# Performance work log

Measured on AMD Instinct MI355X. Metric: run time of the kernel, lower is better.

Reference implementation:

```python
import jax, jax.numpy as jnp
import numpy as np

B, K, BIN = 16, 2048, 256
GRU, EMB, HID = 1024, 1024, 1024
H, KV = 16, 4
D = HID // H          # 64 head dim
NREP = H // KV        # 4 GQA repeat factor


def rotate_half(x):
    x1, x2 = jnp.split(x, 2, axis=-1)
    return jnp.concatenate((-x2, x1), axis=-1)


def setup_inputs() -> dict:
    key = jax.random.key(0)
    ks = jax.random.split(key, 8)
    h = jax.random.normal(ks[0], (B, K, GRU), dtype=jnp.float32)
    # real RoPE frequency tables, shape (BIN, D)
    inv_freq = 1.0 / (10000.0 ** (jnp.arange(0, D, 2, dtype=jnp.float32) / D))
    t = jnp.arange(BIN, dtype=jnp.float32)
    freqs = jnp.outer(t, inv_freq)                      # (BIN, D/2)
    emb = jnp.concatenate((freqs, freqs), axis=-1)      # (BIN, D)
    freqs_cos, freqs_sin = jnp.cos(emb), jnp.sin(emb)
    s = lambda fan: 1.0 / np.sqrt(fan).astype(np.float32)
    Wq = jax.random.normal(ks[1], (H * D, EMB), jnp.float32) * s(EMB)
    Wk = jax.random.normal(ks[2], (KV * D, GRU), jnp.float32) * s(GRU)
    Wv = jax.random.normal(ks[3], (KV * D, GRU), jnp.float32) * s(GRU)
    Wo = jax.random.normal(ks[4], (EMB, H * D), jnp.float32) * s(H * D)
    output_queries = jax.random.normal(ks[5], (BIN, EMB), jnp.float32)
    Wr = jax.random.normal(ks[6], (2, EMB), jnp.float32) * s(EMB)
    br = jnp.zeros((2,), jnp.float32)
    return {"h": h, "freqs_cos": freqs_cos, "freqs_sin": freqs_sin,
            "Wq": Wq, "Wk": Wk, "Wv": Wv, "Wo": Wo,
            "output_queries": output_queries, "Wr": Wr, "br": br}


def reference(h, freqs_cos, freqs_sin, Wq, Wk, Wv, Wo, output_queries, Wr, br):
    # KV projections from GRU history: (B, K, KV, D)
    k = (h @ Wk.T).reshape(B, K, KV, D)
    v = (h @ Wv.T).reshape(B, K, KV, D)
    # Queries are batch-invariant learned tokens: (BIN, H, D)
    q = (output_queries @ Wq.T).reshape(BIN, H, D)
    cos = freqs_cos[:, None, :]  # (BIN, 1, D) broadcast over heads
    sin = freqs_sin[:, None, :]
    q = q * cos + rotate_half(q) * sin
    # GQA: repeat_interleave KV heads to H heads
    k_rep = jnp.repeat(k, NREP, axis=2)  # (B, K, H, D)
    v_rep = jnp.repeat(v, NREP, axis=2)
    scores = jnp.einsum('qhd,bkhd->bhqk', q, k_rep) / np.sqrt(D).astype(np.float32)
    attn = jax.nn.softmax(scores, axis=-1)               # dropout p=0 (eval)
    out = jnp.einsum('bhqk,bkhd->bqhd', attn, v_rep).reshape(B, BIN, H * D)
    z = out @ Wo.T                                        # (B, BIN, EMB)
    return z @ Wr.T + br                                  # (B, BIN, 2)
```

## Files before the change

### kernel.cpp

```cpp
#include <hip/hip_runtime.h>

typedef __attribute__((ext_vector_type(8))) short short8;
typedef __attribute__((ext_vector_type(4))) float f32x4;
typedef __attribute__((ext_vector_type(16))) float f32x16;

#define DEV static __device__ __forceinline__

DEV unsigned short f2bf(float f) {
  unsigned int u = __float_as_uint(f);
  u += 0x7fff + ((u >> 16) & 1);
  return (unsigned short)(u >> 16);
}

DEV unsigned int cvtpk(float lo, float hi) {
  unsigned int r;
  asm("v_cvt_pk_bf16_f32 %0, %1, %2" : "=v"(r) : "v"(lo), "v"(hi));
  return r;
}

DEV float max3f(float a, float b, float c) {
  float r;
  asm("v_max3_f32 %0, %1, %2, %3" : "=v"(r) : "v"(a), "v"(b), "v"(c));
  return r;
}

DEV f32x4 mfma16(short8 a, short8 b, f32x4 c) {
  return __builtin_amdgcn_mfma_f32_16x16x32_bf16(a, b, c, 0, 0, 0);
}

DEV f32x16 mfma32(short8 a, short8 b, f32x16 c) {
  return __builtin_amdgcn_mfma_f32_32x32x16_bf16(a, b, c, 0, 0, 0);
}

DEV void gl_lds16(const void* g, void* l) {
  __builtin_amdgcn_global_load_lds((const __attribute__((address_space(1))) void*)g,
                                   (__attribute__((address_space(3))) void*)l, 16, 0, 0);
}

__global__ __launch_bounds__(256) void cvtB_kernel(const float* __restrict__ Wq,
                                                   const float* __restrict__ Wk,
                                                   const float* __restrict__ Wv,
                                                   unsigned short* __restrict__ wqb,
                                                   unsigned short* __restrict__ wkvb) {
  int id = blockIdx.x * 256 + threadIdx.x;
  int e = id * 4;
  float4 v;
  unsigned short* d;
  if (e < 1048576)      { v = *(const float4*)(Wq + e);             d = wqb + e; }
  else if (e < 1310720) { v = *(const float4*)(Wk + (e - 1048576)); d = wkvb + (e - 1048576); }
  else                  { v = *(const float4*)(Wv + (e - 1310720)); d = wkvb + 262144 + (e - 1310720); }
  uint2 pk;
  pk.x = cvtpk(v.x, v.y);
  pk.y = cvtpk(v.z, v.w);
  *(uint2*)d = pk;
}

__global__ __launch_bounds__(256) void wrp_partial(const float* __restrict__ Wr,
                                                   const float* __restrict__ Wo,
                                                   float* __restrict__ part) {
  int blk = blockIdx.x;
  int tid = threadIdx.x;
  float a0[4] = {0.f,0.f,0.f,0.f};
  float a1[4] = {0.f,0.f,0.f,0.f};
  int e0 = blk * 64;
  for (int e = e0; e < e0 + 64; e++) {
    float w0 = Wr[e];
    float w1 = Wr[1024 + e];
    #pragma unroll
    for (int j4 = 0; j4 < 4; j4++) {
      float wo = Wo[(size_t)e * 1024 + j4 * 256 + tid];
      a0[j4] += w0 * wo;
      a1[j4] += w1 * wo;
    }
  }
  #pragma unroll
  for (int j4 = 0; j4 < 4; j4++) {
    part[blk * 2048 + 0    + j4 * 256 + tid] = a0[j4];
    part[blk * 2048 + 1024 + j4 * 256 + tid] = a1[j4];
  }
}

__global__ __launch_bounds__(256) void wrp_reduce(const float* __restrict__ part,
                                                  float* __restrict__ Wrp) {
  int id = blockIdx.x * 256 + threadIdx.x;
  float s = 0.f;
  #pragma unroll
  for (int blk = 0; blk < 16; blk++) s += part[blk * 2048 + id];
  Wrp[id] = s;
}

__global__ __launch_bounds__(512, 2) void gemm_kv(const float* __restrict__ A,
                                                  const unsigned short* __restrict__ Bb,
                                                  unsigned short* __restrict__ ok,
                                                  unsigned short* __restrict__ vrm) {
  __shared__ unsigned short Asl[3][4096];
  __shared__ unsigned short Bsl[3][16384];

  int bid = blockIdx.x;
  int sw = (bid & 7) * 32 + (bid >> 3);
  int m0 = sw * 128;

  int tid = threadIdx.x;
  int w = tid >> 6, l = tid & 63;
  int l4 = l >> 4, l15 = l & 15;

  int arow = tid >> 2, ac = tid & 3;
  const float* ga = A + (size_t)(m0 + arow) * 1024 + ac * 8;
  int awb = arow * 64 + ((ac ^ ((arow >> 1) & 3)) * 16);

  const unsigned short* gbB = Bb + (size_t)(tid >> 2) * 1024
                                 + (((tid & 3) ^ ((tid >> 3) & 3)) * 8);

  int fsw = (l4 ^ ((l15 >> 1) & 3)) * 16;
  int aoff = l15 * 64 + fsw;
  int boff = (w * 64 + l15) * 64 + fsw;

  f32x4 acc[8][4];
  #pragma unroll
  for (int i = 0; i < 8; i++)
    #pragma unroll
    for (int j = 0; j < 4; j++) acc[i][j] = (f32x4)(0.f);

  float4 aXx, aXy, aYx, aYy;

  #define LOADA(T, RX, RY)                                                  \
    { const float* gA = ga + (T) * 32;                                      \
      RX = *(const float4*)(gA);                                            \
      RY = *(const float4*)(gA + 4); }

  #define STAGEB(SB, T)                                                     \
    { const unsigned short* b0p = gbB + (T) * 32;                           \
      gl_lds16(b0p,          (char*)Bsl[SB] + tid * 16);                    \
      gl_lds16(b0p + 131072, (char*)Bsl[SB] + 8192  + tid * 16);            \
      gl_lds16(b0p + 262144, (char*)Bsl[SB] + 16384 + tid * 16);            \
      gl_lds16(b0p + 393216, (char*)Bsl[SB] + 24576 + tid * 16); }

  #define WRITEA(WB, RX, RY)                                                \
    { union { short8 s; unsigned int u[4]; } af;                            \
      af.u[0] = cvtpk(RX.x, RX.y); af.u[1] = cvtpk(RX.z, RX.w);             \
      af.u[2] = cvtpk(RY.x, RY.y); af.u[3] = cvtpk(RY.z, RY.w);             \
      *(short8*)((char*)Asl[WB] + awb) = af.s; }

  #define COMPUTE(CB)                                                       \
    { const char* Ab = (const char*)Asl[CB];                                \
      const char* Bf = (const char*)Bsl[CB];                                \
      short8 bfr[4];                                                        \
      _Pragma("unroll")                                                     \
      for (int j = 0; j < 4; j++)                                           \
        bfr[j] = *(const short8*)(Bf + boff + j * 1024);                    \
      __builtin_amdgcn_s_setprio(1);                                        \
      _Pragma("unroll")                                                     \
      for (int i = 0; i < 8; i++) {                                         \
        short8 af = *(const short8*)(Ab + aoff + i * 1024);                 \
        _Pragma("unroll")                                                   \
        for (int j = 0; j < 4; j++)                                         \
          acc[i][j] = mfma16(af, bfr[j], acc[i][j]);                        \
      }                                                                     \
      __builtin_amdgcn_s_setprio(0); }

  #define ENDSTEP                                                           \
    { asm volatile("s_waitcnt vmcnt(6)" ::: "memory");                      \
      asm volatile("s_waitcnt lgkmcnt(0)" ::: "memory");                    \
      __builtin_amdgcn_s_barrier();                                         \
      __builtin_amdgcn_sched_barrier(0); }

  LOADA(0, aXx, aXy);
  STAGEB(0, 0);
  WRITEA(0, aXx, aXy);
  LOADA(1, aXx, aXy);
  STAGEB(1, 1);
  asm volatile("s_waitcnt vmcnt(6)" ::: "memory");
  asm volatile("s_waitcnt lgkmcnt(0)" ::: "memory");
  __builtin_amdgcn_s_barrier();
  __builtin_amdgcn_sched_barrier(0);

  #define STEPE(T, CB, WB, SB)                                              \
    { LOADA((T) + 2, aYx, aYy); STAGEB(SB, (T) + 2);                        \
      COMPUTE(CB); WRITEA(WB, aXx, aXy); ENDSTEP }
  #define STEPO(T, CB, WB, SB)                                              \
    { LOADA((T) + 2, aXx, aXy); STAGEB(SB, (T) + 2);                        \
      COMPUTE(CB); WRITEA(WB, aYx, aYy); ENDSTEP }

  #pragma unroll 1
  for (int tb = 0; tb < 30; tb += 6) {
    STEPE(tb + 0, 0, 1, 2);
    STEPO(tb + 1, 1, 2, 0);
    STEPE(tb + 2, 2, 0, 1);
    STEPO(tb + 3, 0, 1, 2);
    STEPE(tb + 4, 1, 2, 0);
    STEPO(tb + 5, 2, 0, 1);
  }
  COMPUTE(0);
  WRITEA(1, aXx, aXy);
  asm volatile("s_waitcnt vmcnt(0)" ::: "memory");
  asm volatile("s_waitcnt lgkmcnt(0)" ::: "memory");
  __builtin_amdgcn_s_barrier();
  __builtin_amdgcn_sched_barrier(0);
  COMPUTE(1);

  #undef LOADA
  #undef STAGEB
  #undef WRITEA
  #undef COMPUTE
  #undef ENDSTEP
  #undef STEPE
  #undef STEPO

  #pragma unroll
  for (int i = 0; i < 8; i++)
    #pragma unroll
    for (int j = 0; j < 4; j++) {
      int n = w * 64 + j * 16 + l15;
      int kvv = n >> 6, d = n & 63;
      #pragma unroll
      for (int r = 0; r < 4; r++) {
        int m = m0 + i * 16 + l4 * 4 + r;
        int bb = m >> 11, kk = m & 2047;
        unsigned short val = f2bf(acc[i][j][r]);
        if (kvv < 4)
          ok[((size_t)(bb * 4 + kvv) * 2048 + kk) * 64 + d] = val;
        else
          vrm[((size_t)(bb * 4 + (kvv - 4)) * 2048 + kk) * 64 + d] = val;
      }
    }
}

__global__ __launch_bounds__(256) void vtr_kernel(const unsigned short* __restrict__ vrm,
                                                  unsigned short* __restrict__ vt) {
  __shared__ unsigned short T[64][72];
  int g = blockIdx.x >> 5;
  int kt = blockIdx.x & 31;
  int tid = threadIdx.x;
  int r = tid >> 2, c0 = (tid & 3) * 16;

  const unsigned short* src = vrm + ((size_t)g * 2048 + kt * 64) * 64;
  *(short8*)&T[r][c0]     = *(const short8*)(src + (size_t)r * 64 + c0);
  *(short8*)&T[r][c0 + 8] = *(const short8*)(src + (size_t)r * 64 + c0 + 8);
  __syncthreads();

  int d = tid >> 2;
  unsigned short* dst = vt + (size_t)g * 131072 + (size_t)d * 2048 + kt * 64 + (tid & 3) * 16;
  short8 o0, o1;
  #pragma unroll
  for (int j = 0; j < 8; j++) {
    o0[j] = (short)T[(tid & 3) * 16 + j][d];
    o1[j] = (short)T[(tid & 3) * 16 + 8 + j][d];
  }
  *(short8*)dst = o0;
  *(short8*)(dst + 8) = o1;
}

__global__ __launch_bounds__(256) void gemm_q(const float* __restrict__ A,
                                              const unsigned short* __restrict__ Bb,
                                              float* __restrict__ of) {
  __shared__ unsigned short Asm[2][4096];
  __shared__ unsigned short Bsm[2][4096];

  int bid = blockIdx.x;
  int ksplit = bid >> 4;
  int m0 = ((bid >> 3) & 1) * 128;
  int n0 = (bid & 7) * 128;
  int t0 = ksplit * 8;
  constexpr int nt = 8;

  int tid = threadIdx.x;
  int w = tid >> 6, l = tid & 63;
  int l4 = l >> 4, l15 = l & 15;
  int wm = w >> 1, wn = w & 1;

  int ra = w * 32 + (l >> 1);
  int rx = (l >> 2) & 3;
  const float* ga = A + (size_t)(m0 + ra) * 1024 + t0 * 32 + (l & 1) * 16;
  int pw0 = (2 * (l & 1) + 0) ^ rx;
  int pw1 = (2 * (l & 1) + 1) ^ rx;
  int awb0 = ra * 64 + pw0 * 16;
  int awb1 = ra * 64 + pw1 * 16;

  int rb = w * 32 + (l >> 2);
  int cb = ((l & 3) ^ ((l >> 3) & 3)) * 8;
  const unsigned short* gb = Bb + (size_t)(n0 + rb) * 1024 + t0 * 32 + cb;

  int qsw = l4 ^ ((l15 >> 1) & 3);
  int arb = (wm * 64 + l15) * 64 + qsw * 16;
  int brb = (wn * 64 + l15) * 64 + qsw * 16;

  f32x4 acc[4][4];
  #pragma unroll
  for (int i = 0; i < 4; i++)
    #pragma unroll
    for (int j = 0; j < 4; j++) acc[i][j] = (f32x4)(0.f);

  float4 fa0, fa1, fa2, fa3;

  #define LOADA(tt)                                                        \
    { const float* gA = ga + (tt) * 32;                                    \
      fa0 = *(const float4*)(gA);                                          \
      fa1 = *(const float4*)(gA + 4);                                      \
      fa2 = *(const float4*)(gA + 8);                                      \
      fa3 = *(const float4*)(gA + 12); }

  #define WRITEA(bufi)                                                     \
    { union { short8 s; unsigned int u[4]; } t0u, t1u;                     \
      t0u.u[0] = cvtpk(fa0.x, fa0.y); t0u.u[1] = cvtpk(fa0.z, fa0.w);      \
      t0u.u[2] = cvtpk(fa1.x, fa1.y); t0u.u[3] = cvtpk(fa1.z, fa1.w);      \
      t1u.u[0] = cvtpk(fa2.x, fa2.y); t1u.u[1] = cvtpk(fa2.z, fa2.w);      \
      t1u.u[2] = cvtpk(fa3.x, fa3.y); t1u.u[3] = cvtpk(fa3.z, fa3.w);      \
      *(short8*)((char*)Asm[bufi] + awb0) = t0u.s;                         \
      *(short8*)((char*)Asm[bufi] + awb1) = t1u.s; }

  #define STAGEB(bufi, tt)                                                 \
    { char* lb = (char*)Bsm[bufi] + w * 2048;                              \
      const unsigned short* gB = gb + (tt) * 32;                           \
      gl_lds16(gB, lb);                                                    \
      gl_lds16(gB + 16384, lb + 1024); }

  LOADA(0);
  STAGEB(0, 0);
  WRITEA(0);
  __syncthreads();

  for (int t = 0; t < nt; t++) {
    int buf = t & 1;
    if (t + 1 < nt) {
      LOADA(t + 1);
      STAGEB(buf ^ 1, t + 1);
    }
    short8 af[4], bfg[4];
    #pragma unroll
    for (int i = 0; i < 4; i++)
      af[i] = *(const short8*)((char*)Asm[buf] + arb + i * 1024);
    #pragma unroll
    for (int j = 0; j < 4; j++)
      bfg[j] = *(const short8*)((char*)Bsm[buf] + brb + j * 1024);
    #pragma unroll
    for (int i = 0; i < 4; i++)
      #pragma unroll
      for (int j = 0; j < 4; j++)
        acc[i][j] = mfma16(af[i], bfg[j], acc[i][j]);
    if (t + 1 < nt) WRITEA(buf ^ 1);
    __syncthreads();
  }
  #undef LOADA
  #undef WRITEA
  #undef STAGEB

  float* o = of + (size_t)ksplit * 262144;
  #pragma unroll
  for (int i = 0; i < 4; i++)
    #pragma unroll
    for (int j = 0; j < 4; j++) {
      int n = n0 + wn * 64 + j * 16 + l15;
      #pragma unroll
      for (int r = 0; r < 4; r++) {
        int m = m0 + wm * 64 + i * 16 + l4 * 4 + r;
        o[(size_t)m * 1024 + n] = acc[i][j][r];
      }
    }
}

__global__ __launch_bounds__(256) void rope_kernel(const float* __restrict__ qp,
                                                   const float* __restrict__ cosb,
                                                   const float* __restrict__ sinb,
                                                   unsigned short* __restrict__ qb) {
  int id = blockIdx.x * 256 + threadIdx.x;
  int qrow = id >> 10, hd = id & 1023, hh = hd >> 6, d = hd & 63;
  int od = hh * 64 + ((d < 32) ? d + 32 : d - 32);
  float v = 0.f, o = 0.f;
  #pragma unroll
  for (int s4 = 0; s4 < 4; s4++) {
    v += qp[s4 * 262144 + qrow * 1024 + hd];
    o += qp[s4 * 262144 + qrow * 1024 + od];
  }
  if (d < 32) o = -o;
  float c = cosb[qrow * 64 + d];
  float s = sinb[qrow * 64 + d];
  float outv = (v * c + o * s) * 0.18033688011112042f;
  qb[((size_t)hh * 256 + qrow) * 64 + d] = f2bf(outv);
}

__global__ __launch_bounds__(256) void attn_kernel(const unsigned short* __restrict__ qb,
                                                   const unsigned short* __restrict__ kb,
                                                   const unsigned short* __restrict__ vb,
                                                   const float* __restrict__ Wrp,
                                                   float* __restrict__ part) {
  __shared__ unsigned short Kt[2][4096];
  __shared__ unsigned short Vt[2][4096];

  int bid = blockIdx.x;
  int x = bid & 7, mid = (bid >> 3) & 7, top2 = bid >> 6;
  int g = mid * 8 + x;
  int b = g >> 2, kvh = g & 3;
  int split = top2 >> 3;
  int top = top2 & 7;
  int hl = top >> 1, qh = top & 1;
  int h = kvh * 4 + hl;

  int tid = threadIdx.x;
  int w = tid >> 6, l = tid & 63;
  int q31 = l & 31, L = l >> 5;
  int qg = qh * 128 + w * 32 + q31;

  const unsigned short* kg = kb + (size_t)(b * 4 + kvh) * 2048 * 64;
  const unsigned short* vg = vb + (size_t)(b * 4 + kvh) * 64 * 2048;

  short8 qf[4];
  #pragma unroll
  for (int c = 0; c < 4; c++)
    qf[c] = *(const short8*)&qb[((size_t)h * 256 + qg) * 64 + c * 16 + L * 8];

  f32x16 Ot[2];
  Ot[0] = (f32x16)(0.f); Ot[1] = (f32x16)(0.f);
  float m = -1e30f, lsum = 0.f;

  int ksrow = tid >> 3, kslot = tid & 7;
  const unsigned short* ksrc = kg + (size_t)ksrow * 64 + ((kslot ^ (ksrow & 7)) * 8);
  int vsrow = tid >> 2, vslot = tid & 3;
  const unsigned short* vsrc = vg + (size_t)vsrow * 2048 + ((vslot ^ ((vsrow >> 1) & 3)) * 8);

  int tb0 = split * 16;

  #define STAGE(bufi, tt)                                                       \
    { gl_lds16(ksrc + (size_t)((tt) * 2 + 0) * 2048, (char*)Kt[bufi] + tid * 16);        \
      gl_lds16(ksrc + (size_t)((tt) * 2 + 1) * 2048, (char*)Kt[bufi] + 4096 + tid * 16); \
      gl_lds16(vsrc + ((tt) * 2 + 0) * 32,           (char*)Vt[bufi] + tid * 16);        \
      gl_lds16(vsrc + ((tt) * 2 + 1) * 32,           (char*)Vt[bufi] + 4096 + tid * 16); }

  STAGE(0, tb0);
  __syncthreads();

  for (int t = 0; t < 16; t++) {
    int buf = t & 1;
    if (t + 1 < 16) STAGE(buf ^ 1, tb0 + t + 1);

    #pragma unroll
    for (int sub = 0; sub < 2; sub++) {
      const char* Kb = (const char*)Kt[buf] + sub * 4096;
      const char* Vb = (const char*)Vt[buf] + sub * 4096;

      f32x16 st = (f32x16)(0.f);
      #pragma unroll
      for (int c = 0; c < 4; c++) {
        int row = q31;
        int byt = row * 128 + (((c * 2 + L) ^ (row & 7)) * 16);
        short8 kf = *(const short8*)(Kb + byt);
        st = mfma32(kf, qf[c], st);
      }

      float g0 = max3f(st[0], st[1], st[2]);
      float g1 = max3f(st[3], st[4], st[5]);
      float g2 = max3f(st[6], st[7], st[8]);
      float g3 = max3f(st[9], st[10], st[11]);
      float g4 = max3f(st[12], st[13], st[14]);
      float mx = fmaxf(max3f(g0, g1, g2), max3f(g3, g4, st[15]));
      mx = fmaxf(mx, __shfl_xor(mx, 32));

      if (!__all(mx <= m + 8.f)) {
        float mnew = fmaxf(m, mx);
        float corr = exp2f(m - mnew);
        lsum *= corr;
        #pragma unroll
        for (int db = 0; db < 2; db++)
          #pragma unroll
          for (int r = 0; r < 16; r++) Ot[db][r] *= corr;
        m = mnew;
      }

      float p[16];
      float ls = 0.f;
      #pragma unroll
      for (int r = 0; r < 16; r++) {
        p[r] = exp2f(st[r] - m);
        ls += p[r];
      }
      lsum += ls;

      unsigned int pw[2][4];
      #pragma unroll
      for (int kc = 0; kc < 2; kc++) {
        unsigned int A0 = cvtpk(p[kc * 8 + 0], p[kc * 8 + 1]);
        unsigned int A1 = cvtpk(p[kc * 8 + 2], p[kc * 8 + 3]);
        unsigned int B0 = cvtpk(p[kc * 8 + 4], p[kc * 8 + 5]);
        unsigned int B1 = cvtpk(p[kc * 8 + 6], p[kc * 8 + 7]);
        asm volatile("v_permlane32_swap_b32 %0, %1" : "+v"(A0), "+v"(B0));
        asm volatile("v_permlane32_swap_b32 %0, %1" : "+v"(A1), "+v"(B1));
        pw[kc][0] = A0; pw[kc][1] = A1; pw[kc][2] = B0; pw[kc][3] = B1;
      }

      #pragma unroll
      for (int db = 0; db < 2; db++) {
        int drow = db * 32 + q31;
        #pragma unroll
        for (int kc = 0; kc < 2; kc++) {
          int byt = drow * 64 + (((kc * 2 + L) ^ ((drow >> 1) & 3)) * 16);
          short8 vf = *(const short8*)(Vb + byt);
          short8 pf;
          {
            union { short8 s; unsigned int u[4]; } uu;
            uu.u[0] = pw[kc][0]; uu.u[1] = pw[kc][1];
            uu.u[2] = pw[kc][2]; uu.u[3] = pw[kc][3];
            pf = uu.s;
          }
          Ot[db] = mfma32(vf, pf, Ot[db]);
        }
      }
    }

    __syncthreads();
  }
  #undef STAGE

  lsum += __shfl_xor(lsum, 32);

  float a0 = 0.f, a1 = 0.f;
  #pragma unroll
  for (int db = 0; db < 2; db++)
    #pragma unroll
    for (int rq = 0; rq < 4; rq++) {
      int dbase = db * 32 + rq * 8 + L * 4;
      float4 w0v = *(const float4*)(Wrp + h * 64 + dbase);
      float4 w1v = *(const float4*)(Wrp + 1024 + h * 64 + dbase);
      #pragma unroll
      for (int j = 0; j < 4; j++) {
        float o = Ot[db][rq * 4 + j];
        a0 += o * ((const float*)&w0v)[j];
        a1 += o * ((const float*)&w1v)[j];
      }
    }
  a0 += __shfl_xor(a0, 32);
  a1 += __shfl_xor(a1, 32);

  if (L == 0) {
    size_t base = ((((size_t)(b * 16 + h) * 256 + qg) * 2) + split) * 4;
    float4 r4;
    r4.x = m; r4.y = lsum; r4.z = a0; r4.w = a1;
    *(float4*)&part[base] = r4;
  }
}

__global__ __launch_bounds__(256) void final_kernel(const float* __restrict__ part,
                                                    const float* __restrict__ br,
                                                    float* __restrict__ out) {
  int id = blockIdx.x * 256 + threadIdx.x;
  int c = id & 1, q = (id >> 1) & 255, b = id >> 9;
  float s = br[c];
  #pragma unroll
  for (int hh = 0; hh < 16; hh++) {
    size_t base = (((size_t)(b * 16 + hh) * 256 + q) * 2) * 4;
    float4 f0 = *(const float4*)&part[base];
    float4 f1 = *(const float4*)&part[base + 4];
    float mm = fmaxf(f0.x, f1.x);
    float w0 = exp2f(f0.x - mm), w1 = exp2f(f1.x - mm);
    float den = w0 * f0.y + w1 * f1.y;
    float num = (c == 0) ? (w0 * f0.z + w1 * f1.z) : (w0 * f0.w + w1 * f1.w);
    s += num / den;
  }
  out[id] = s;
}

extern "C" void kernel_launch(void* const* d_in, const int* in_sizes, int n_in,
                              void* d_out, int out_size, void* d_ws, size_t ws_size,
                              hipStream_t stream) {
  const float* h    = (const float*)d_in[0];
  const float* fcos = (const float*)d_in[1];
  const float* fsin = (const float*)d_in[2];
  const float* Wq   = (const float*)d_in[3];
  const float* Wk   = (const float*)d_in[4];
  const float* Wv   = (const float*)d_in[5];
  const float* Wo   = (const float*)d_in[6];
  const float* oq   = (const float*)d_in[7];
  const float* Wr   = (const float*)d_in[8];
  const float* br   = (const float*)d_in[9];
  float* out = (float*)d_out;

  char* ws = (char*)d_ws;
  unsigned short* kbuf = (unsigned short*)(ws);
  unsigned short* vbuf = (unsigned short*)(ws + 16777216);
  float* qpart         = (float*)(ws + 33554432);
  unsigned short* qbf  = (unsigned short*)(ws + 37748736);
  float* wpart         = (float*)(ws + 38273024);
  float* Wrp           = (float*)(ws + 38404096);
  float* apart         = (float*)(ws + 38412288);
  unsigned short* wqb  = (unsigned short*)(ws + 42606592);
  unsigned short* wkvb = (unsigned short*)(ws + 44703744);
  unsigned short* vrm  = (unsigned short*)(ws + 45752320);

  cvtB_kernel<<<dim3(1536), dim3(256), 0, stream>>>(Wq, Wk, Wv, wqb, wkvb);
  wrp_partial<<<dim3(16), dim3(256), 0, stream>>>(Wr, Wo, wpart);
  wrp_reduce<<<dim3(8), dim3(256), 0, stream>>>(wpart, Wrp);
  gemm_q<<<dim3(64), dim3(256), 0, stream>>>(oq, wqb, qpart);
  rope_kernel<<<dim3(1024), dim3(256), 0, stream>>>(qpart, fcos, fsin, qbf);
  gemm_kv<<<dim3(256), dim3(512), 0, stream>>>(h, wkvb, kbuf, vrm);
  vtr_kernel<<<dim3(2048), dim3(256), 0, stream>>>(vrm, vbuf);
  attn_kernel<<<dim3(1024), dim3(256), 0, stream>>>(qbf, kbuf, vbuf, Wrp, apart);
  final_kernel<<<dim3(32), dim3(256), 0, stream>>>(apart, br, out);
}
```

Baseline: 152.3 us.

## Triple-buffer K/V tiles with vmcnt-based waits in attention kernel

Switches the attention kernel's K/V shared-memory staging from double to triple buffering. It keeps two tiles of global-to-LDS loads in flight and replaces the per-iteration __syncthreads with an explicit s_waitcnt vmcnt(8) plus s_barrier. The aim is to hide global load latency behind MFMA/softmax compute. This raises LDS usage, which may reduce occupancy, and correctness now depends on the hand-counted outstanding-load accounting.

Result: faster. 147.6 us, median of 2 (-3.0%).

```diff
diff --git a/kernel.cpp b/kernel.cpp
--- a/kernel.cpp
+++ b/kernel.cpp
@@ -383,8 +383,8 @@
                                                    const unsigned short* __restrict__ vb,
                                                    const float* __restrict__ Wrp,
                                                    float* __restrict__ part) {
-  __shared__ unsigned short Kt[2][4096];
-  __shared__ unsigned short Vt[2][4096];
+  __shared__ unsigned short Kt[3][4096];
+  __shared__ unsigned short Vt[3][4096];
 
   int bid = blockIdx.x;
   int x = bid & 7, mid = (bid >> 3) & 7, top2 = bid >> 6;
@@ -425,89 +425,102 @@
       gl_lds16(vsrc + ((tt) * 2 + 0) * 32,           (char*)Vt[bufi] + tid * 16);        \
       gl_lds16(vsrc + ((tt) * 2 + 1) * 32,           (char*)Vt[bufi] + 4096 + tid * 16); }
 
-  STAGE(0, tb0);
-  __syncthreads();
-
-  for (int t = 0; t < 16; t++) {
-    int buf = t & 1;
-    if (t + 1 < 16) STAGE(buf ^ 1, tb0 + t + 1);
-
-    #pragma unroll
-    for (int sub = 0; sub < 2; sub++) {
-      const char* Kb = (const char*)Kt[buf] + sub * 4096;
-      const char* Vb = (const char*)Vt[buf] + sub * 4096;
-
-      f32x16 st = (f32x16)(0.f);
-      #pragma unroll
-      for (int c = 0; c < 4; c++) {
-        int row = q31;
-        int byt = row * 128 + (((c * 2 + L) ^ (row & 7)) * 16);
-        short8 kf = *(const short8*)(Kb + byt);
-        st = mfma32(kf, qf[c], st);
-      }
-
-      float g0 = max3f(st[0], st[1], st[2]);
-      float g1 = max3f(st[3], st[4], st[5]);
-      float g2 = max3f(st[6], st[7], st[8]);
-      float g3 = max3f(st[9], st[10], st[11]);
-      float g4 = max3f(st[12], st[13], st[14]);
-      float mx = fmaxf(max3f(g0, g1, g2), max3f(g3, g4, st[15]));
-      mx = fmaxf(mx, __shfl_xor(mx, 32));
-
-      if (!__all(mx <= m + 8.f)) {
-        float mnew = fmaxf(m, mx);
-        float corr = exp2f(m - mnew);
-        lsum *= corr;
-        #pragma unroll
-        for (int db = 0; db < 2; db++)
-          #pragma unroll
-          for (int r = 0; r < 16; r++) Ot[db][r] *= corr;
-        m = mnew;
-      }
-
-      float p[16];
-      float ls = 0.f;
-      #pragma unroll
-      for (int r = 0; r < 16; r++) {
-        p[r] = exp2f(st[r] - m);
-        ls += p[r];
-      }
-      lsum += ls;
-
-      unsigned int pw[2][4];
-      #pragma unroll
-      for (int kc = 0; kc < 2; kc++) {
-        unsigned int A0 = cvtpk(p[kc * 8 + 0], p[kc * 8 + 1]);
-        unsigned int A1 = cvtpk(p[kc * 8 + 2], p[kc * 8 + 3]);
-        unsigned int B0 = cvtpk(p[kc * 8 + 4], p[kc * 8 + 5]);
-        unsigned int B1 = cvtpk(p[kc * 8 + 6], p[kc * 8 + 7]);
-        asm volatile("v_permlane32_swap_b32 %0, %1" : "+v"(A0), "+v"(B0));
-        asm volatile("v_permlane32_swap_b32 %0, %1" : "+v"(A1), "+v"(B1));
-        pw[kc][0] = A0; pw[kc][1] = A1; pw[kc][2] = B0; pw[kc][3] = B1;
-      }
-
-      #pragma unroll
-      for (int db = 0; db < 2; db++) {
-        int drow = db * 32 + q31;
-        #pragma unroll
-        for (int kc = 0; kc < 2; kc++) {
-          int byt = drow * 64 + (((kc * 2 + L) ^ ((drow >> 1) & 3)) * 16);
-          short8 vf = *(const short8*)(Vb + byt);
-          short8 pf;
-          {
-            union { short8 s; unsigned int u[4]; } uu;
-            uu.u[0] = pw[kc][0]; uu.u[1] = pw[kc][1];
-            uu.u[2] = pw[kc][2]; uu.u[3] = pw[kc][3];
-            pf = uu.s;
-          }
-          Ot[db] = mfma32(vf, pf, Ot[db]);
-        }
-      }
+  #define COMPUTE(CB)                                                           \
+    _Pragma("unroll")                                                           \
+    for (int sub = 0; sub < 2; sub++) {                                         \
+      const char* Kb = (const char*)Kt[CB] + sub * 4096;                        \
+      const char* Vb = (const char*)Vt[CB] + sub * 4096;                        \
+      f32x16 st = (f32x16)(0.f);                                                \
+      _Pragma("unroll")                                                         \
+      for (int c = 0; c < 4; c++) {                                             \
+        int row = q31;                                                          \
+        int byt = row * 128 + (((c * 2 + L) ^ (row & 7)) * 16);                 \
+        short8 kf = *(const short8*)(Kb + byt);                                 \
+        st = mfma32(kf, qf[c], st);                                             \
+      }                                                                         \
+      float g0 = max3f(st[0], st[1], st[2]);                                    \
+      float g1 = max3f(st[3], st[4], st[5]);                                    \
+      float g2 = max3f(st[6], st[7], st[8]);                                    \
+      float g3 = max3f(st[9], st[10], st[11]);                                  \
+      float g4 = max3f(st[12], st[13], st[14]);                                 \
+      float mx = fmaxf(max3f(g0, g1, g2), max3f(g3, g4, st[15]));               \
+      mx = fmaxf(mx, __shfl_xor(mx, 32));                                       \
+      if (!__all(mx <= m + 8.f)) {                                              \
+        float mnew = fmaxf(m, mx);                                              \
+        float corr = exp2f(m - mnew);                                           \
+        lsum *= corr;                                                           \
+        _Pragma("unroll")                                                       \
+        for (int db = 0; db < 2; db++)                                          \
+          _Pragma("unroll")                                                     \
+          for (int r = 0; r < 16; r++) Ot[db][r] *= corr;                       \
+        m = mnew;                                                               \
+      }                                                                         \
+      float p[16];                                                              \
+      float ls = 0.f;                                                           \
+      _Pragma("unroll")                                                         \
+      for (int r = 0; r < 16; r++) {                                            \
+        p[r] = exp2f(st[r] - m);                                                \
+        ls += p[r];                                                             \
+      }                                                                         \
+      lsum += ls;                                                               \
+      unsigned int pw[2][4];                                                    \
+      _Pragma("unroll")                                                         \
+      for (int kc = 0; kc < 2; kc++) {                                          \
+        unsigned int A0 = cvtpk(p[kc * 8 + 0], p[kc * 8 + 1]);                  \
+        unsigned int A1 = cvtpk(p[kc * 8 + 2], p[kc * 8 + 3]);                  \
+        unsigned int B0 = cvtpk(p[kc * 8 + 4], p[kc * 8 + 5]);                  \
+        unsigned int B1 = cvtpk(p[kc * 8 + 6], p[kc * 8 + 7]);                  \
+        asm volatile("v_permlane32_swap_b32 %0, %1" : "+v"(A0), "+v"(B0));      \
+        asm volatile("v_permlane32_swap_b32 %0, %1" : "+v"(A1), "+v"(B1));      \
+        pw[kc][0] = A0; pw[kc][1] = A1; pw[kc][2] = B0; pw[kc][3] = B1;         \
+      }                                                                         \
+      _Pragma("unroll")                                                         \
+      for (int db = 0; db < 2; db++) {                                          \
+        int drow = db * 32 + q31;                                               \
+        _Pragma("unroll")                                                       \
+        for (int kc = 0; kc < 2; kc++) {                                        \
+          int byt = drow * 64 + (((kc * 2 + L) ^ ((drow >> 1) & 3)) * 16);      \
+          short8 vf = *(const short8*)(Vb + byt);                               \
+          short8 pf;                                                            \
+          {                                                                     \
+            union { short8 s; unsigned int u[4]; } uu;                          \
+            uu.u[0] = pw[kc][0]; uu.u[1] = pw[kc][1];                           \
+            uu.u[2] = pw[kc][2]; uu.u[3] = pw[kc][3];                           \
+            pf = uu.s;                                                          \
+          }                                                                     \
+          Ot[db] = mfma32(vf, pf, Ot[db]);                                      \
+        }                                                                       \
+      }                                                                         \
     }
 
-    __syncthreads();
-  }
+  #define E8                                                                    \
+    { asm volatile("s_waitcnt vmcnt(8)" ::: "memory");                          \
+      __builtin_amdgcn_s_barrier();                                             \
+      __builtin_amdgcn_sched_barrier(0); }
+
+  STAGE(0, tb0 + 0);
+  STAGE(1, tb0 + 1);
+  asm volatile("s_waitcnt vmcnt(8)" ::: "memory");
+  __builtin_amdgcn_s_barrier();
+  __builtin_amdgcn_sched_barrier(0);
+
+  #pragma unroll 1
+  for (int tb = 0; tb < 12; tb += 3) {
+    STAGE(2, tb0 + tb + 2); COMPUTE(0) E8;
+    STAGE(0, tb0 + tb + 3); COMPUTE(1) E8;
+    STAGE(1, tb0 + tb + 4); COMPUTE(2) E8;
+  }
+  STAGE(2, tb0 + 14); COMPUTE(0) E8;
+  STAGE(0, tb0 + 15); COMPUTE(1) E8;
+  COMPUTE(2)
+  asm volatile("s_waitcnt vmcnt(0)" ::: "memory");
+  __builtin_amdgcn_s_barrier();
+  __builtin_amdgcn_sched_barrier(0);
+  COMPUTE(0)
+
   #undef STAGE
+  #undef COMPUTE
+  #undef E8
 
   lsum += __shfl_xor(lsum, 32);
 
```
